# Optimization experiments

Hardware: AMD Instinct MI355X
Metric: run time of the kernel (lower is better)

Reference implementation:

```python
import jax, jax.numpy as jnp
import numpy as np

D_MODEL = 256
N_HEADS = 8
D_K = 16
LN_EPS = 1e-5


def setup_inputs() -> dict:
    key = jax.random.key(0)
    ks = jax.random.split(key, 10)
    B, S = 4, 2048
    inp = {
        "input_Q": jax.random.normal(ks[0], (B, S, D_MODEL), dtype=jnp.float32),
        "input_K": jax.random.normal(ks[1], (B, S, D_MODEL), dtype=jnp.float32),
        "input_V": jax.random.normal(ks[2], (B, S, D_MODEL), dtype=jnp.float32),
        "attn_mask": jax.random.randint(ks[3], (B, S, S), 0, 2) == 1,
        # learned params (torch Linear weight [out,in] stored here as [in,out])
        "Wq": jax.random.normal(ks[4], (D_MODEL, N_HEADS * D_K), dtype=jnp.float32) * (1.0 / np.sqrt(D_MODEL)),
        "Wk": jax.random.normal(ks[5], (D_MODEL, N_HEADS * D_K), dtype=jnp.float32) * (1.0 / np.sqrt(D_MODEL)),
        "Wv": jax.random.normal(ks[6], (D_MODEL, N_HEADS * D_K), dtype=jnp.float32) * (1.0 / np.sqrt(D_MODEL)),
        "Wfc": jax.random.normal(ks[7], (N_HEADS * D_K, D_MODEL), dtype=jnp.float32) * (1.0 / np.sqrt(N_HEADS * D_K)),
        "ln_gamma": jnp.ones((D_MODEL,), dtype=jnp.float32),
        "ln_beta": jnp.zeros((D_MODEL,), dtype=jnp.float32),
    }
    return inp


def reference(input_Q, input_K, input_V, attn_mask, Wq, Wk, Wv, Wfc, ln_gamma, ln_beta):
    B, S, _ = input_Q.shape
    # projections -> [B, H, S, d_k]
    Q = (input_Q @ Wq).reshape(B, S, N_HEADS, D_K).transpose(0, 2, 1, 3)
    K = (input_K @ Wk).reshape(B, S, N_HEADS, D_K).transpose(0, 2, 1, 3)
    V = (input_V @ Wv).reshape(B, S, N_HEADS, D_K).transpose(0, 2, 1, 3)
    # scores [B, H, S, S], masked softmax
    scores = jnp.einsum("bhqd,bhkd->bhqk", Q, K) / np.sqrt(D_K).astype(np.float32)
    scores = jnp.where(attn_mask[:, None, :, :], jnp.float32(-1e9), scores)
    attn = jax.nn.softmax(scores, axis=-1)
    context = jnp.einsum("bhqk,bhkd->bhqd", attn, V)
    context = context.transpose(0, 2, 1, 3).reshape(B, S, N_HEADS * D_K)
    out = context @ Wfc
    # LayerNorm (no residual in the original module)
    mu = jnp.mean(out, axis=-1, keepdims=True)
    var = jnp.var(out, axis=-1, keepdims=True)
    out = (out - mu) * jax.lax.rsqrt(var + LN_EPS) * ln_gamma + ln_beta
    return out
```

## Files before the change

### kernel.cpp

```cpp
#include <hip/hip_runtime.h>
#include <hip/hip_bf16.h>

#define S_LEN 2048
#define BATCH 4
#define NH 8
#define DK 16
#define DM 256
#define DP 128
#define L2E 1.4426950408889634f

typedef short bf16x8 __attribute__((ext_vector_type(8)));
typedef short short4v __attribute__((ext_vector_type(4)));
typedef float f32x16 __attribute__((ext_vector_type(16)));

__device__ __forceinline__ short f2bf(float x) {
    __hip_bfloat16 h = __float2bfloat16(x);
    return __builtin_bit_cast(short, h);
}

union Frag { bf16x8 v; short4v h2[2]; };

__global__ __launch_bounds__(256) void phase1(
    const void* __restrict__ mraw,
    unsigned long long* __restrict__ ms64,
    const float* __restrict__ Xq, const float* __restrict__ Xk, const float* __restrict__ Xv,
    const float* __restrict__ Wq, const float* __restrict__ Wk, const float* __restrict__ Wv,
    short* __restrict__ Qt, short* __restrict__ Kb, short* __restrict__ Vb)
{
    __shared__ short xs_s[32 * 260];
    __shared__ int isBool;
    const int bi = blockIdx.x;
    const int t = threadIdx.x;

    if (bi < 768) {
        const int inp = bi >> 8;
        const int s0 = (bi & 255) * 32;
        {
            const float* xbase = ((inp == 0) ? Xq : (inp == 1) ? Xk : Xv) + (size_t)s0 * 256;
            #pragma unroll
            for (int u = 0; u < 8; ++u) {
                const int idx = u * 1024 + t * 4;
                const int row = idx >> 8, col = idx & 255;
                float4 xv = *(const float4*)(xbase + idx);
                short4v o = { f2bf(xv.x), f2bf(xv.y), f2bf(xv.z), f2bf(xv.w) };
                *(short4v*)&xs_s[row * 260 + col] = o;
            }
        }
        __syncthreads();

        const int wave = t >> 6, lane = t & 63;
        const int lq = lane & 31, hi = lane >> 5;
        const int c = wave * 32 + lq;

        const float* W = (inp == 0) ? Wq : (inp == 1) ? Wk : Wv;
        const float scale = (inp == 0) ? 0.25f * L2E : 1.0f;
        Frag wf[16];
        #pragma unroll
        for (int kb = 0; kb < 16; ++kb) {
            const int k0 = kb * 16 + 4 * hi;
            union { bf16x8 v; short s[8]; } o;
            #pragma unroll
            for (int e = 0; e < 4; ++e) {
                o.s[e]     = f2bf(W[(size_t)(k0 + e) * DP + c] * scale);
                o.s[4 + e] = f2bf(W[(size_t)(k0 + 8 + e) * DP + c] * scale);
            }
            wf[kb].v = o.v;
        }

        f32x16 acc;
        #pragma unroll
        for (int i = 0; i < 16; ++i) acc[i] = 0.f;

        #pragma unroll
        for (int kb = 0; kb < 16; ++kb) {
            Frag af;
            af.h2[0] = *(const short4v*)&xs_s[lq * 260 + kb*16 + 4*hi];
            af.h2[1] = *(const short4v*)&xs_s[lq * 260 + kb*16 + 8 + 4*hi];
            acc = __builtin_amdgcn_mfma_f32_32x32x16_bf16(af.v, wf[kb].v, acc, 0, 0, 0);
        }

        const int b = s0 >> 11, sl = s0 & (S_LEN - 1);
        const int h = c >> 4, d = c & 15;
        if (inp == 1) {
            #pragma unroll
            for (int r = 0; r < 16; ++r) {
                const int s = sl + (r & 3) + 8*(r >> 2) + 4*hi;
                Kb[(((size_t)(b * NH + h)) * S_LEN + s) * DK + d] = f2bf(acc[r]);
            }
        } else {
            short* base = (inp == 0)
                ? Qt + (((size_t)(b * NH + h)) * 16 + d) * S_LEN + sl
                : Vb + (((size_t)(b * NH + h)) * 32 + d) * S_LEN + sl;
            #pragma unroll
            for (int g = 0; g < 4; ++g) {
                short4v vv = { f2bf(acc[4*g]), f2bf(acc[4*g+1]), f2bf(acc[4*g+2]), f2bf(acc[4*g+3]) };
                *(short4v*)(base + 8*g + 4*hi) = vv;
            }
        }
    } else if (bi < 1280) {
        const int tid = (bi - 768) * 256 + t;
        const int bh = tid >> 12;
        const int rem = tid & 4095;
        const int row = 16 + (rem >> 11) * 4;
        const int s = rem & 2047;
        Vb[((size_t)bh * 32 + row) * S_LEN + s] = (short)0x3F80;
    } else {
        const size_t kbase0 = (size_t)(bi - 1280) * 4096;
        if (t == 0) isBool = 0;
        __syncthreads();
        {
            unsigned int u = ((const unsigned int*)mraw)[(kbase0 >> 2) + t * 4];
            if (u & 0xFFFFFF00u) isBool = 1;
        }
        __syncthreads();

        const int lane = t & 63;
        const size_t kbase = kbase0 + (size_t)(t >> 6) * 1024;
        int v[16];
        if (!isBool) {
            const int* p = (const int*)mraw + kbase + lane;
            #pragma unroll
            for (int g = 0; g < 16; ++g) v[g] = p[g * 64];
        } else {
            const unsigned char* p = (const unsigned char*)mraw + kbase + lane;
            #pragma unroll
            for (int g = 0; g < 16; ++g) v[g] = p[g * 64];
        }

        const size_t row = kbase >> 11;
        const int koff0 = (int)(kbase & 2047);

        #pragma unroll
        for (int g = 0; g < 16; ++g) {
            const unsigned long long W = __ballot(v[g] != 0);
            if (lane == 0) {
                const int koff = koff0 + g * 64;
                ms64[(size_t)(koff >> 7) * (BATCH*S_LEN*2) + row*2 + ((koff >> 6) & 1)] = W;
            }
        }
    }
}

__global__ __launch_bounds__(256, 8) void attn_mfma(
    const short* __restrict__ Qt, const short* __restrict__ Kb, const short* __restrict__ Vb,
    const unsigned long long* __restrict__ ms64, float* __restrict__ pacc, float* __restrict__ pl)
{
    __shared__ short kt_s[128 * 20];
    __shared__ short vt_s[32 * 132];

    const int bh = blockIdx.y;
    const int b = bh >> 3;
    const int z = blockIdx.z;
    const int t = threadIdx.x;
    const int wave = t >> 6, lane = t & 63;
    const int lq = lane & 31, hi = lane >> 5;
    const int qrow = blockIdx.x * 128 + wave * 32 + lq;

    Frag qf;
    {
        const short* qt = Qt + (size_t)bh * 16 * S_LEN + qrow;
        #pragma unroll
        for (int j = 0; j < 4; ++j) {
            qf.h2[0][j] = qt[(size_t)(4*hi + j) * S_LEN];
            qf.h2[1][j] = qt[(size_t)(8 + 4*hi + j) * S_LEN];
        }
    }

    f32x16 acc;
    #pragma unroll
    for (int i = 0; i < 16; ++i) acc[i] = 0.f;

    const short* kbase = Kb + (size_t)bh * S_LEN * DK;
    const short* vbase = Vb + (size_t)bh * 32 * S_LEN;
    const unsigned long long* mbase = ms64 + ((size_t)b * S_LEN + qrow) * 2;

    const int tiles = (S_LEN / 128) / gridDim.z;
    const int t0 = z * tiles, t1 = t0 + tiles;

    for (int tile = t0; tile < t1; ++tile) {
        const int k0 = tile * 128;

        {
            const uint4 kv = *(const uint4*)(kbase + (size_t)k0 * DK + t * 8);
            short* kdst = &kt_s[(t >> 1) * 20 + (t & 1) * 8];
            *(uint2*)(kdst)     = *(uint2*)&kv;
            *(uint2*)(kdst + 4) = *((uint2*)&kv + 1);

            const short* vsrc = vbase + (size_t)(t >> 3) * S_LEN + k0 + (t & 7) * 16;
            uint4 v0 = *(const uint4*)(vsrc);
            uint4 v1 = *(const uint4*)(vsrc + 8);
            short* vdst = &vt_s[(t >> 3) * 132 + (t & 7) * 16];
            *(uint2*)(vdst)      = *(uint2*)&v0;
            *(uint2*)(vdst + 4)  = *((uint2*)&v0 + 1);
            *(uint2*)(vdst + 8)  = *(uint2*)&v1;
            *(uint2*)(vdst + 12) = *((uint2*)&v1 + 1);
        }
        __syncthreads();

        const unsigned long long* mw = mbase + (size_t)tile * (BATCH * S_LEN * 2);
        const unsigned long long W64a = mw[0], W64b = mw[1];

        #pragma unroll
        for (int kt = 0; kt < 4; ++kt) {
            const unsigned int W = (unsigned int)(((kt < 2) ? W64a : W64b)
                                                  >> (32*(kt & 1) + 4*hi));
            f32x16 ci;
            #pragma unroll
            for (int r = 0; r < 16; ++r) {
                const int bit = (r & 3) + 8*(r >> 2);
                ci[r] = __int_as_float(((int)(W << (31 - bit)) >> 31) & 0xC2C80000);
            }

            Frag kf;
            kf.h2[0] = *(const short4v*)&kt_s[(kt*32 + lq) * 20 + 4*hi];
            kf.h2[1] = *(const short4v*)&kt_s[(kt*32 + lq) * 20 + 8 + 4*hi];
            f32x16 p = __builtin_amdgcn_mfma_f32_32x32x16_bf16(kf.v, qf.v, ci, 0, 0, 0);

            #pragma unroll
            for (int r = 0; r < 16; ++r) p[r] = __builtin_amdgcn_exp2f(p[r]);

            #pragma unroll
            for (int j = 0; j < 2; ++j) {
                union { bf16x8 v; unsigned int u[4]; } pf;
                #pragma unroll
                for (int e = 0; e < 4; ++e) {
                    asm("v_cvt_pk_bf16_f32 %0, %1, %2"
                        : "=v"(pf.u[e]) : "v"(p[j*8 + 2*e]), "v"(p[j*8 + 2*e + 1]));
                }
                Frag vf;
                const int vo = lq * 132 + (kt*2 + j) * 16 + 4*hi;
                vf.h2[0] = *(const short4v*)&vt_s[vo];
                vf.h2[1] = *(const short4v*)&vt_s[vo + 8];
                acc = __builtin_amdgcn_mfma_f32_32x32x16_bf16(vf.v, pf.v, acc, 0, 0, 0);
            }
        }
        __syncthreads();
    }

    float* pb = pacc + (((size_t)z * (BATCH*NH) + bh) * S_LEN + qrow) * 16;
    float4 o1 = { acc[0], acc[1], acc[2], acc[3] };
    float4 o2 = { acc[4], acc[5], acc[6], acc[7] };
    *(float4*)(pb + 4*hi) = o1;
    *(float4*)(pb + 8 + 4*hi) = o2;
    if (hi == 0) pl[((size_t)z * (BATCH*NH) + bh) * S_LEN + qrow] = acc[8];
}

__global__ __launch_bounds__(256) void fc_ln(
    const float* __restrict__ pacc, const float* __restrict__ pl, int ns,
    const float* __restrict__ Wfc,
    const float* __restrict__ gamma, const float* __restrict__ beta,
    float* __restrict__ out)
{
    __shared__ float cs[8][DP];
    __shared__ float ys[8][256];
    __shared__ float red[16];
    const int t = threadIdx.x;
    const int row0 = blockIdx.x * 8;

    {
        const int idx = t * 4;
        const int r = idx >> 7, k = idx & 127;
        const int grow = row0 + r;
        const int b = grow >> 11, q = grow & (S_LEN - 1);
        const int h = k >> 4, d0 = k & 15;
        float4 s = {0.f, 0.f, 0.f, 0.f};
        float L = 0.f;
        for (int z = 0; z < ns; ++z) {
            const size_t o = ((size_t)z * (BATCH*NH) + b * NH + h) * S_LEN + q;
            const float4 a = *(const float4*)(pacc + o * 16 + d0);
            s.x += a.x; s.y += a.y; s.z += a.z; s.w += a.w;
            L += pl[o];
        }
        const float inv = 1.0f / L;
        float4 o4 = { s.x * inv, s.y * inv, s.z * inv, s.w * inv };
        *(float4*)&cs[r][k] = o4;
    }
    __syncthreads();

    float acc[8] = {0,0,0,0,0,0,0,0};
    for (int k = 0; k < DP; k += 4) {
        const float w0 = Wfc[(k+0)*DM + t];
        const float w1 = Wfc[(k+1)*DM + t];
        const float w2 = Wfc[(k+2)*DM + t];
        const float w3 = Wfc[(k+3)*DM + t];
        #pragma unroll
        for (int r = 0; r < 8; ++r) {
            float4 x = *(const float4*)&cs[r][k];
            acc[r] = fmaf(x.x, w0, fmaf(x.y, w1, fmaf(x.z, w2, fmaf(x.w, w3, acc[r]))));
        }
    }

    #pragma unroll
    for (int r = 0; r < 8; ++r) ys[r][t] = acc[r];
    __syncthreads();

    const int w = t >> 6, lj = t & 63;
    #pragma unroll
    for (int rr = 0; rr < 2; ++rr) {
        const int r = w * 2 + rr;
        float a0 = ys[r][lj], a1 = ys[r][lj+64], a2 = ys[r][lj+128], a3 = ys[r][lj+192];
        float s1 = a0 + a1 + a2 + a3;
        float s2 = a0*a0 + a1*a1 + a2*a2 + a3*a3;
        #pragma unroll
        for (int off = 32; off; off >>= 1) {
            s1 += __shfl_xor(s1, off);
            s2 += __shfl_xor(s2, off);
        }
        if (lj == 0) {
            float mu = s1 * (1.0f/256.0f);
            float var = s2 * (1.0f/256.0f) - mu*mu;
            red[r*2]     = mu;
            red[r*2 + 1] = rsqrtf(var + 1e-5f);
        }
    }
    __syncthreads();

    const float g = gamma[t], be = beta[t];
    #pragma unroll
    for (int r = 0; r < 8; ++r) {
        float y = (acc[r] - red[r*2]) * red[r*2 + 1];
        out[(size_t)(row0 + r) * DM + t] = fmaf(y, g, be);
    }
}

extern "C" void kernel_launch(void* const* d_in, const int* in_sizes, int n_in,
                              void* d_out, int out_size, void* d_ws, size_t ws_size,
                              hipStream_t stream)
{
    const float* Xq = (const float*)d_in[0];
    const float* Xk = (const float*)d_in[1];
    const float* Xv = (const float*)d_in[2];
    const void* mask_raw = d_in[3];
    const float* Wq  = (const float*)d_in[4];
    const float* Wk  = (const float*)d_in[5];
    const float* Wv  = (const float*)d_in[6];
    const float* Wfc = (const float*)d_in[7];
    const float* gamma = (const float*)d_in[8];
    const float* beta  = (const float*)d_in[9];
    float* out = (float*)d_out;

    const size_t headsz = (size_t)BATCH * NH * S_LEN * DK;
    const size_t maskelems = (size_t)BATCH * S_LEN * S_LEN;

    char* wsb = (char*)d_ws;
    short* Qt = (short*)wsb;
    short* Kb = Qt + headsz;
    short* Vb = Kb + headsz;
    unsigned long long* msk = (unsigned long long*)(Vb + 2 * headsz);
    float* pacc = (float*)(msk + maskelems / 64);
    size_t ns = 4;
    {
        const size_t fixed = (size_t)((char*)pacc - wsb);
        while (ns > 1 && fixed + ns * ((size_t)BATCH*NH*S_LEN*17*4) > ws_size)
            ns >>= 1;
    }
    float* pl = pacc + ns * (size_t)BATCH * NH * S_LEN * 16;

    phase1<<<dim3(768 + 512 + (unsigned)(maskelems / 4096)), dim3(256), 0, stream>>>(
        mask_raw, msk, Xq, Xk, Xv, Wq, Wk, Wv, Qt, Kb, Vb);
    attn_mfma<<<dim3(S_LEN / 128, BATCH * NH, (unsigned)ns), dim3(256), 0, stream>>>(
        Qt, Kb, Vb, msk, pacc, pl);
    fc_ln<<<dim3(BATCH * S_LEN / 8), dim3(256), 0, stream>>>(pacc, pl, (int)ns, Wfc, gamma, beta, out);
}
```

Measured before the change: 72.44 us.

## Pre-pack bf16 weight fragments, split projection kernel, row-major mask bit layout

Moves weight conversion into a prep kernel that writes pre-scaled bf16 MFMA fragments once, so the projection blocks load 16-byte fragments instead of 128 scattered fp32 reads each. The projection GEMM becomes its own kernel launched after prep, which adds one launch. The mask bitmap is rearranged to per-query-row contiguous 64-bit words, written with coalesced stores from 16 lanes and read in attention as a single 16-byte load per tile. The trade-off is an extra kernel boundary and serialization between mask/weight prep and projection.

Result: no change. 72.85 us (+0.6%).

```diff
diff --git a/kernel.cpp b/kernel.cpp
--- a/kernel.cpp
+++ b/kernel.cpp
@@ -20,92 +20,41 @@
 
 union Frag { bf16x8 v; short4v h2[2]; };
 
-__global__ __launch_bounds__(256) void phase1(
-    const void* __restrict__ mraw,
-    unsigned long long* __restrict__ ms64,
-    const float* __restrict__ Xq, const float* __restrict__ Xk, const float* __restrict__ Xv,
-    const float* __restrict__ Wq, const float* __restrict__ Wk, const float* __restrict__ Wv,
-    short* __restrict__ Qt, short* __restrict__ Kb, short* __restrict__ Vb)
-{
-    __shared__ short xs_s[32 * 260];
+__global__ __launch_bounds__(256) void prep(
+    const void* __restrict__ mraw, unsigned long long* __restrict__ ms64,
+    const float* __restrict__ Wq, const float* __restrict__ Wk,
+    const float* __restrict__ Wv, short* __restrict__ Wt,
+    short* __restrict__ Vb)
+{
     __shared__ int isBool;
     const int bi = blockIdx.x;
     const int t = threadIdx.x;
 
-    if (bi < 768) {
-        const int inp = bi >> 8;
-        const int s0 = (bi & 255) * 32;
-        {
-            const float* xbase = ((inp == 0) ? Xq : (inp == 1) ? Xk : Xv) + (size_t)s0 * 256;
-            #pragma unroll
-            for (int u = 0; u < 8; ++u) {
-                const int idx = u * 1024 + t * 4;
-                const int row = idx >> 8, col = idx & 255;
-                float4 xv = *(const float4*)(xbase + idx);
-                short4v o = { f2bf(xv.x), f2bf(xv.y), f2bf(xv.z), f2bf(xv.w) };
-                *(short4v*)&xs_s[row * 260 + col] = o;
-            }
-        }
-        __syncthreads();
-
-        const int wave = t >> 6, lane = t & 63;
-        const int lq = lane & 31, hi = lane >> 5;
-        const int c = wave * 32 + lq;
-
-        const float* W = (inp == 0) ? Wq : (inp == 1) ? Wk : Wv;
-        const float scale = (inp == 0) ? 0.25f * L2E : 1.0f;
-        Frag wf[16];
-        #pragma unroll
-        for (int kb = 0; kb < 16; ++kb) {
-            const int k0 = kb * 16 + 4 * hi;
-            union { bf16x8 v; short s[8]; } o;
-            #pragma unroll
-            for (int e = 0; e < 4; ++e) {
-                o.s[e]     = f2bf(W[(size_t)(k0 + e) * DP + c] * scale);
-                o.s[4 + e] = f2bf(W[(size_t)(k0 + 8 + e) * DP + c] * scale);
-            }
-            wf[kb].v = o.v;
-        }
-
-        f32x16 acc;
-        #pragma unroll
-        for (int i = 0; i < 16; ++i) acc[i] = 0.f;
-
-        #pragma unroll
-        for (int kb = 0; kb < 16; ++kb) {
-            Frag af;
-            af.h2[0] = *(const short4v*)&xs_s[lq * 260 + kb*16 + 4*hi];
-            af.h2[1] = *(const short4v*)&xs_s[lq * 260 + kb*16 + 8 + 4*hi];
-            acc = __builtin_amdgcn_mfma_f32_32x32x16_bf16(af.v, wf[kb].v, acc, 0, 0, 0);
-        }
-
-        const int b = s0 >> 11, sl = s0 & (S_LEN - 1);
-        const int h = c >> 4, d = c & 15;
-        if (inp == 1) {
-            #pragma unroll
-            for (int r = 0; r < 16; ++r) {
-                const int s = sl + (r & 3) + 8*(r >> 2) + 4*hi;
-                Kb[(((size_t)(b * NH + h)) * S_LEN + s) * DK + d] = f2bf(acc[r]);
-            }
-        } else {
-            short* base = (inp == 0)
-                ? Qt + (((size_t)(b * NH + h)) * 16 + d) * S_LEN + sl
-                : Vb + (((size_t)(b * NH + h)) * 32 + d) * S_LEN + sl;
-            #pragma unroll
-            for (int g = 0; g < 4; ++g) {
-                short4v vv = { f2bf(acc[4*g]), f2bf(acc[4*g+1]), f2bf(acc[4*g+2]), f2bf(acc[4*g+3]) };
-                *(short4v*)(base + 8*g + 4*hi) = vv;
-            }
-        }
-    } else if (bi < 1280) {
-        const int tid = (bi - 768) * 256 + t;
+    if (bi < 512) {
+        const int tid = bi * 256 + t;
         const int bh = tid >> 12;
         const int rem = tid & 4095;
         const int row = 16 + (rem >> 11) * 4;
         const int s = rem & 2047;
         Vb[((size_t)bh * 32 + row) * S_LEN + s] = (short)0x3F80;
+    } else if (bi < 560) {
+        const int tid = (bi - 512) * 256 + t;
+        const int c  = tid & 127;
+        const int hi = (tid >> 7) & 1;
+        const int kb = (tid >> 8) & 15;
+        const int m  = tid >> 12;
+        const float* W = (m == 0) ? Wq : (m == 1) ? Wk : Wv;
+        const float scale = (m == 0) ? 0.25f * L2E : 1.0f;
+        const int k0 = kb * 16 + 4 * hi;
+        union { bf16x8 v; short s[8]; } o;
+        #pragma unroll
+        for (int e = 0; e < 4; ++e) {
+            o.s[e]     = f2bf(W[(size_t)(k0 + e) * DP + c] * scale);
+            o.s[4 + e] = f2bf(W[(size_t)(k0 + 8 + e) * DP + c] * scale);
+        }
+        *(bf16x8*)(Wt + (size_t)tid * 8) = o.v;
     } else {
-        const size_t kbase0 = (size_t)(bi - 1280) * 4096;
+        const size_t kbase0 = (size_t)(bi - 560) * 4096;
         if (t == 0) isBool = 0;
         __syncthreads();
         {
@@ -128,15 +77,81 @@
         }
 
         const size_t row = kbase >> 11;
-        const int koff0 = (int)(kbase & 2047);
-
+        const int w0 = (int)(kbase & 2047) >> 6;
+
+        unsigned long long myw = 0;
         #pragma unroll
         for (int g = 0; g < 16; ++g) {
             const unsigned long long W = __ballot(v[g] != 0);
-            if (lane == 0) {
-                const int koff = koff0 + g * 64;
-                ms64[(size_t)(koff >> 7) * (BATCH*S_LEN*2) + row*2 + ((koff >> 6) & 1)] = W;
-            }
+            myw = (lane == g) ? W : myw;
+        }
+        if (lane < 16) ms64[row * 32 + w0 + lane] = myw;
+    }
+}
+
+__global__ __launch_bounds__(256) void proj_mfma(
+    const float* __restrict__ Xq, const float* __restrict__ Xk, const float* __restrict__ Xv,
+    const short* __restrict__ Wt,
+    short* __restrict__ Qt, short* __restrict__ Kb, short* __restrict__ Vb)
+{
+    __shared__ short xs_s[32 * 260];
+    const int bi = blockIdx.x;
+    const int t = threadIdx.x;
+    const int inp = bi >> 8;
+    const int s0 = (bi & 255) * 32;
+
+    {
+        const float* xbase = ((inp == 0) ? Xq : (inp == 1) ? Xk : Xv) + (size_t)s0 * 256;
+        #pragma unroll
+        for (int u = 0; u < 8; ++u) {
+            const int idx = u * 1024 + t * 4;
+            const int row = idx >> 8, col = idx & 255;
+            float4 xv = *(const float4*)(xbase + idx);
+            short4v o = { f2bf(xv.x), f2bf(xv.y), f2bf(xv.z), f2bf(xv.w) };
+            *(short4v*)&xs_s[row * 260 + col] = o;
+        }
+    }
+
+    const int wave = t >> 6, lane = t & 63;
+    const int lq = lane & 31, hi = lane >> 5;
+    const int c = wave * 32 + lq;
+
+    const short* w2 = Wt + (((size_t)inp * 16 * 2 + hi) * 128 + c) * 8;
+    Frag wf[16];
+    #pragma unroll
+    for (int kb = 0; kb < 16; ++kb)
+        wf[kb].v = *(const bf16x8*)(w2 + (size_t)kb * 2048);
+    asm volatile("" ::: "memory");
+    __syncthreads();
+
+    f32x16 acc;
+    #pragma unroll
+    for (int i = 0; i < 16; ++i) acc[i] = 0.f;
+
+    #pragma unroll
+    for (int kb = 0; kb < 16; ++kb) {
+        Frag af;
+        af.h2[0] = *(const short4v*)&xs_s[lq * 260 + kb*16 + 4*hi];
+        af.h2[1] = *(const short4v*)&xs_s[lq * 260 + kb*16 + 8 + 4*hi];
+        acc = __builtin_amdgcn_mfma_f32_32x32x16_bf16(af.v, wf[kb].v, acc, 0, 0, 0);
+    }
+
+    const int b = s0 >> 11, sl = s0 & (S_LEN - 1);
+    const int h = c >> 4, d = c & 15;
+    if (inp == 1) {
+        #pragma unroll
+        for (int r = 0; r < 16; ++r) {
+            const int s = sl + (r & 3) + 8*(r >> 2) + 4*hi;
+            Kb[(((size_t)(b * NH + h)) * S_LEN + s) * DK + d] = f2bf(acc[r]);
+        }
+    } else {
+        short* base = (inp == 0)
+            ? Qt + (((size_t)(b * NH + h)) * 16 + d) * S_LEN + sl
+            : Vb + (((size_t)(b * NH + h)) * 32 + d) * S_LEN + sl;
+        #pragma unroll
+        for (int g = 0; g < 4; ++g) {
+            short4v vv = { f2bf(acc[4*g]), f2bf(acc[4*g+1]), f2bf(acc[4*g+2]), f2bf(acc[4*g+3]) };
+            *(short4v*)(base + 8*g + 4*hi) = vv;
         }
     }
 }
@@ -172,7 +187,7 @@
 
     const short* kbase = Kb + (size_t)bh * S_LEN * DK;
     const short* vbase = Vb + (size_t)bh * 32 * S_LEN;
-    const unsigned long long* mbase = ms64 + ((size_t)b * S_LEN + qrow) * 2;
+    const unsigned long long* mrow = ms64 + ((size_t)b * S_LEN + qrow) * 32;
 
     const int tiles = (S_LEN / 128) / gridDim.z;
     const int t0 = z * tiles, t1 = t0 + tiles;
@@ -197,8 +212,8 @@
         }
         __syncthreads();
 
-        const unsigned long long* mw = mbase + (size_t)tile * (BATCH * S_LEN * 2);
-        const unsigned long long W64a = mw[0], W64b = mw[1];
+        const ulonglong2 mw = *(const ulonglong2*)(mrow + tile * 2);
+        const unsigned long long W64a = mw.x, W64b = mw.y;
 
         #pragma unroll
         for (int kt = 0; kt < 4; ++kt) {
@@ -347,7 +362,8 @@
     short* Kb = Qt + headsz;
     short* Vb = Kb + headsz;
     unsigned long long* msk = (unsigned long long*)(Vb + 2 * headsz);
-    float* pacc = (float*)(msk + maskelems / 64);
+    short* Wt = (short*)(msk + maskelems / 64);
+    float* pacc = (float*)(Wt + 3 * 128 * 256);
     size_t ns = 4;
     {
         const size_t fixed = (size_t)((char*)pacc - wsb);
@@ -356,8 +372,9 @@
     }
     float* pl = pacc + ns * (size_t)BATCH * NH * S_LEN * 16;
 
-    phase1<<<dim3(768 + 512 + (unsigned)(maskelems / 4096)), dim3(256), 0, stream>>>(
-        mask_raw, msk, Xq, Xk, Xv, Wq, Wk, Wv, Qt, Kb, Vb);
+    prep<<<dim3(512 + 48 + (unsigned)(maskelems / 4096)), dim3(256), 0, stream>>>(
+        mask_raw, msk, Wq, Wk, Wv, Wt, Vb);
+    proj_mfma<<<dim3(768), dim3(256), 0, stream>>>(Xq, Xk, Xv, Wt, Qt, Kb, Vb);
     attn_mfma<<<dim3(S_LEN / 128, BATCH * NH, (unsigned)ns), dim3(256), 0, stream>>>(
         Qt, Kb, Vb, msk, pacc, pl);
     fc_ln<<<dim3(BATCH * S_LEN / 8), dim3(256), 0, stream>>>(pacc, pl, (int)ns, Wfc, gamma, beta, out);
```

## Split key range across block halves and combine partial softmax in LDS

Applied to the files above, without the earlier changes.

The attention kernel now runs 512 threads per block. The two 256-thread halves each process half of the key tiles with their own LDS buffers, and their partial accumulators and row sums are combined through shared memory. The normalized context is written directly, so the partial-accumulator buffers and the reduction in fc_ln are no longer needed. The mask bitmap layout changes to row-major, so each query row loads its two words with one 16-byte load, and the ballot results are written by 16 lanes at once instead of one store per group. A syncthreads in the projection is moved after the weight loads. The trade-off is fewer blocks per CU (launch bounds 512,4), less key-split parallelism (2 instead of up to 4), and extra block-wide barriers.

New measurement: 93.90 us. +29.6%, slower.

```diff
diff --git a/kernel.cpp b/kernel.cpp
--- a/kernel.cpp
+++ b/kernel.cpp
@@ -20,9 +20,8 @@
 
 union Frag { bf16x8 v; short4v h2[2]; };
 
-__global__ __launch_bounds__(256) void phase1(
-    const void* __restrict__ mraw,
-    unsigned long long* __restrict__ ms64,
+__global__ __launch_bounds__(256) void main1(
+    const void* __restrict__ mraw, unsigned long long* __restrict__ ms64,
     const float* __restrict__ Xq, const float* __restrict__ Xk, const float* __restrict__ Xv,
     const float* __restrict__ Wq, const float* __restrict__ Wk, const float* __restrict__ Wv,
     short* __restrict__ Qt, short* __restrict__ Kb, short* __restrict__ Vb)
@@ -46,7 +45,6 @@
                 *(short4v*)&xs_s[row * 260 + col] = o;
             }
         }
-        __syncthreads();
 
         const int wave = t >> 6, lane = t & 63;
         const int lq = lane & 31, hi = lane >> 5;
@@ -66,6 +64,7 @@
             }
             wf[kb].v = o.v;
         }
+        __syncthreads();
 
         f32x16 acc;
         #pragma unroll
@@ -128,33 +127,35 @@
         }
 
         const size_t row = kbase >> 11;
-        const int koff0 = (int)(kbase & 2047);
-
+        const int w0 = (int)(kbase & 2047) >> 6;
+
+        unsigned long long myw = 0;
         #pragma unroll
         for (int g = 0; g < 16; ++g) {
             const unsigned long long W = __ballot(v[g] != 0);
-            if (lane == 0) {
-                const int koff = koff0 + g * 64;
-                ms64[(size_t)(koff >> 7) * (BATCH*S_LEN*2) + row*2 + ((koff >> 6) & 1)] = W;
-            }
-        }
-    }
-}
-
-__global__ __launch_bounds__(256, 8) void attn_mfma(
+            myw = (lane == g) ? W : myw;
+        }
+        if (lane < 16) ms64[row * 32 + w0 + lane] = myw;
+    }
+}
+
+__global__ __launch_bounds__(512, 4) void attn_mfma(
     const short* __restrict__ Qt, const short* __restrict__ Kb, const short* __restrict__ Vb,
-    const unsigned long long* __restrict__ ms64, float* __restrict__ pacc, float* __restrict__ pl)
+    const unsigned long long* __restrict__ ms64, float* __restrict__ ctx)
 {
-    __shared__ short kt_s[128 * 20];
-    __shared__ short vt_s[32 * 132];
+    __shared__ short kt_s[2][128 * 20];
+    __shared__ short vt_s[2][32 * 132];
+    __shared__ float cmb[256][9];
 
     const int bh = blockIdx.y;
-    const int b = bh >> 3;
-    const int z = blockIdx.z;
+    const int b = bh >> 3, h = bh & 7;
     const int t = threadIdx.x;
-    const int wave = t >> 6, lane = t & 63;
+    const int half = t >> 8;
+    const int th = t & 255;
+    const int wv = (t >> 6) & 3;
+    const int lane = t & 63;
     const int lq = lane & 31, hi = lane >> 5;
-    const int qrow = blockIdx.x * 128 + wave * 32 + lq;
+    const int qrow = blockIdx.x * 128 + wv * 32 + lq;
 
     Frag qf;
     {
@@ -172,24 +173,22 @@
 
     const short* kbase = Kb + (size_t)bh * S_LEN * DK;
     const short* vbase = Vb + (size_t)bh * 32 * S_LEN;
-    const unsigned long long* mbase = ms64 + ((size_t)b * S_LEN + qrow) * 2;
-
-    const int tiles = (S_LEN / 128) / gridDim.z;
-    const int t0 = z * tiles, t1 = t0 + tiles;
-
-    for (int tile = t0; tile < t1; ++tile) {
+    const unsigned long long* mrow = ms64 + ((size_t)b * S_LEN + qrow) * 32;
+
+    for (int i = 0; i < 8; ++i) {
+        const int tile = half * 8 + i;
         const int k0 = tile * 128;
 
         {
-            const uint4 kv = *(const uint4*)(kbase + (size_t)k0 * DK + t * 8);
-            short* kdst = &kt_s[(t >> 1) * 20 + (t & 1) * 8];
+            const uint4 kv = *(const uint4*)(kbase + (size_t)k0 * DK + th * 8);
+            short* kdst = &kt_s[half][(th >> 1) * 20 + (th & 1) * 8];
             *(uint2*)(kdst)     = *(uint2*)&kv;
             *(uint2*)(kdst + 4) = *((uint2*)&kv + 1);
 
-            const short* vsrc = vbase + (size_t)(t >> 3) * S_LEN + k0 + (t & 7) * 16;
+            const short* vsrc = vbase + (size_t)(th >> 3) * S_LEN + k0 + (th & 7) * 16;
             uint4 v0 = *(const uint4*)(vsrc);
             uint4 v1 = *(const uint4*)(vsrc + 8);
-            short* vdst = &vt_s[(t >> 3) * 132 + (t & 7) * 16];
+            short* vdst = &vt_s[half][(th >> 3) * 132 + (th & 7) * 16];
             *(uint2*)(vdst)      = *(uint2*)&v0;
             *(uint2*)(vdst + 4)  = *((uint2*)&v0 + 1);
             *(uint2*)(vdst + 8)  = *(uint2*)&v1;
@@ -197,8 +196,8 @@
         }
         __syncthreads();
 
-        const unsigned long long* mw = mbase + (size_t)tile * (BATCH * S_LEN * 2);
-        const unsigned long long W64a = mw[0], W64b = mw[1];
+        const ulonglong2 mw = *(const ulonglong2*)(mrow + tile * 2);
+        const unsigned long long W64a = mw.x, W64b = mw.y;
 
         #pragma unroll
         for (int kt = 0; kt < 4; ++kt) {
@@ -212,8 +211,8 @@
             }
 
             Frag kf;
-            kf.h2[0] = *(const short4v*)&kt_s[(kt*32 + lq) * 20 + 4*hi];
-            kf.h2[1] = *(const short4v*)&kt_s[(kt*32 + lq) * 20 + 8 + 4*hi];
+            kf.h2[0] = *(const short4v*)&kt_s[half][(kt*32 + lq) * 20 + 4*hi];
+            kf.h2[1] = *(const short4v*)&kt_s[half][(kt*32 + lq) * 20 + 8 + 4*hi];
             f32x16 p = __builtin_amdgcn_mfma_f32_32x32x16_bf16(kf.v, qf.v, ci, 0, 0, 0);
 
             #pragma unroll
@@ -229,25 +228,34 @@
                 }
                 Frag vf;
                 const int vo = lq * 132 + (kt*2 + j) * 16 + 4*hi;
-                vf.h2[0] = *(const short4v*)&vt_s[vo];
-                vf.h2[1] = *(const short4v*)&vt_s[vo + 8];
+                vf.h2[0] = *(const short4v*)&vt_s[half][vo];
+                vf.h2[1] = *(const short4v*)&vt_s[half][vo + 8];
                 acc = __builtin_amdgcn_mfma_f32_32x32x16_bf16(vf.v, pf.v, acc, 0, 0, 0);
             }
         }
         __syncthreads();
     }
 
-    float* pb = pacc + (((size_t)z * (BATCH*NH) + bh) * S_LEN + qrow) * 16;
-    float4 o1 = { acc[0], acc[1], acc[2], acc[3] };
-    float4 o2 = { acc[4], acc[5], acc[6], acc[7] };
-    *(float4*)(pb + 4*hi) = o1;
-    *(float4*)(pb + 8 + 4*hi) = o2;
-    if (hi == 0) pl[((size_t)z * (BATCH*NH) + bh) * S_LEN + qrow] = acc[8];
+    if (half == 1) {
+        #pragma unroll
+        for (int e = 0; e < 8; ++e) cmb[th][e] = acc[e];
+        cmb[th][8] = acc[8];
+    }
+    __syncthreads();
+    if (half == 0) {
+        const float invl = 1.0f / (acc[8] + cmb[th][8]);
+        float* cbase = ctx + ((size_t)b * S_LEN + qrow) * DP + h * DK;
+        float4 o1 = { (acc[0] + cmb[th][0]) * invl, (acc[1] + cmb[th][1]) * invl,
+                      (acc[2] + cmb[th][2]) * invl, (acc[3] + cmb[th][3]) * invl };
+        float4 o2 = { (acc[4] + cmb[th][4]) * invl, (acc[5] + cmb[th][5]) * invl,
+                      (acc[6] + cmb[th][6]) * invl, (acc[7] + cmb[th][7]) * invl };
+        *(float4*)(cbase + 4*hi) = o1;
+        *(float4*)(cbase + 8 + 4*hi) = o2;
+    }
 }
 
 __global__ __launch_bounds__(256) void fc_ln(
-    const float* __restrict__ pacc, const float* __restrict__ pl, int ns,
-    const float* __restrict__ Wfc,
+    const float* __restrict__ ctx, const float* __restrict__ Wfc,
     const float* __restrict__ gamma, const float* __restrict__ beta,
     float* __restrict__ out)
 {
@@ -260,20 +268,7 @@
     {
         const int idx = t * 4;
         const int r = idx >> 7, k = idx & 127;
-        const int grow = row0 + r;
-        const int b = grow >> 11, q = grow & (S_LEN - 1);
-        const int h = k >> 4, d0 = k & 15;
-        float4 s = {0.f, 0.f, 0.f, 0.f};
-        float L = 0.f;
-        for (int z = 0; z < ns; ++z) {
-            const size_t o = ((size_t)z * (BATCH*NH) + b * NH + h) * S_LEN + q;
-            const float4 a = *(const float4*)(pacc + o * 16 + d0);
-            s.x += a.x; s.y += a.y; s.z += a.z; s.w += a.w;
-            L += pl[o];
-        }
-        const float inv = 1.0f / L;
-        float4 o4 = { s.x * inv, s.y * inv, s.z * inv, s.w * inv };
-        *(float4*)&cs[r][k] = o4;
+        *(float4*)&cs[r][k] = *(const float4*)(ctx + (size_t)(row0 + r) * DP + k);
     }
     __syncthreads();
 
@@ -347,18 +342,11 @@
     short* Kb = Qt + headsz;
     short* Vb = Kb + headsz;
     unsigned long long* msk = (unsigned long long*)(Vb + 2 * headsz);
-    float* pacc = (float*)(msk + maskelems / 64);
-    size_t ns = 4;
-    {
-        const size_t fixed = (size_t)((char*)pacc - wsb);
-        while (ns > 1 && fixed + ns * ((size_t)BATCH*NH*S_LEN*17*4) > ws_size)
-            ns >>= 1;
-    }
-    float* pl = pacc + ns * (size_t)BATCH * NH * S_LEN * 16;
-
-    phase1<<<dim3(768 + 512 + (unsigned)(maskelems / 4096)), dim3(256), 0, stream>>>(
+    float* ctx = (float*)(msk + maskelems / 64);
+
+    main1<<<dim3(768 + 512 + (unsigned)(maskelems / 4096)), dim3(256), 0, stream>>>(
         mask_raw, msk, Xq, Xk, Xv, Wq, Wk, Wv, Qt, Kb, Vb);
-    attn_mfma<<<dim3(S_LEN / 128, BATCH * NH, (unsigned)ns), dim3(256), 0, stream>>>(
-        Qt, Kb, Vb, msk, pacc, pl);
-    fc_ln<<<dim3(BATCH * S_LEN / 8), dim3(256), 0, stream>>>(pacc, pl, (int)ns, Wfc, gamma, beta, out);
-}
+    attn_mfma<<<dim3(S_LEN / 128, BATCH * NH), dim3(512), 0, stream>>>(
+        Qt, Kb, Vb, msk, ctx);
+    fc_ln<<<dim3(BATCH * S_LEN / 8), dim3(256), 0, stream>>>(ctx, Wfc, gamma, beta, out);
+}
```

## Pack mask bits with vector loads and row-major bitmask layout

Applied to the files above, without the earlier changes.

Mask compression now has each lane load 16 contiguous bytes with one vector load and pack them into 16 bits with multiply tricks, then uses shuffles to assemble 64-bit words. The packed-mask layout changes from tile-major to row-major, so the attention kernel reads both words for a tile with a single 16-byte load. The projection block also moves its barrier after the weight-fragment loads so those global loads overlap with the shared-memory staging. The bool-detection probe changes to check the loaded data itself, and the int path now reads 16 contiguous ints per lane, which is less coalesced.

New measurement: 71.32 us. Within noise of the previous version (-1.6%).

```diff
diff --git a/kernel.cpp b/kernel.cpp
--- a/kernel.cpp
+++ b/kernel.cpp
@@ -20,9 +20,8 @@
 
 union Frag { bf16x8 v; short4v h2[2]; };
 
-__global__ __launch_bounds__(256) void phase1(
-    const void* __restrict__ mraw,
-    unsigned long long* __restrict__ ms64,
+__global__ __launch_bounds__(256) void main1(
+    const void* __restrict__ mraw, unsigned long long* __restrict__ ms64,
     const float* __restrict__ Xq, const float* __restrict__ Xk, const float* __restrict__ Xv,
     const float* __restrict__ Wq, const float* __restrict__ Wk, const float* __restrict__ Wv,
     short* __restrict__ Qt, short* __restrict__ Kb, short* __restrict__ Vb)
@@ -46,7 +45,6 @@
                 *(short4v*)&xs_s[row * 260 + col] = o;
             }
         }
-        __syncthreads();
 
         const int wave = t >> 6, lane = t & 63;
         const int lq = lane & 31, hi = lane >> 5;
@@ -66,6 +64,7 @@
             }
             wf[kb].v = o.v;
         }
+        __syncthreads();
 
         f32x16 acc;
         #pragma unroll
@@ -105,38 +104,45 @@
         const int s = rem & 2047;
         Vb[((size_t)bh * 32 + row) * S_LEN + s] = (short)0x3F80;
     } else {
+        const int lane = t & 63;
         const size_t kbase0 = (size_t)(bi - 1280) * 4096;
+        const size_t kbase = kbase0 + (size_t)(t >> 6) * 1024;
+
+        union { uint4 v; unsigned u[4]; } uu;
+        uu.v = *(const uint4*)((const unsigned char*)mraw + kbase + 16 * lane);
+
         if (t == 0) isBool = 0;
         __syncthreads();
-        {
-            unsigned int u = ((const unsigned int*)mraw)[(kbase0 >> 2) + t * 4];
-            if (u & 0xFFFFFF00u) isBool = 1;
-        }
-        __syncthreads();
-
-        const int lane = t & 63;
-        const size_t kbase = kbase0 + (size_t)(t >> 6) * 1024;
-        int v[16];
-        if (!isBool) {
-            const int* p = (const int*)mraw + kbase + lane;
-            #pragma unroll
-            for (int g = 0; g < 16; ++g) v[g] = p[g * 64];
+        if ((uu.u[0] | uu.u[1] | uu.u[2] | uu.u[3]) & 0xFFFFFF00u) isBool = 1;
+        __syncthreads();
+
+        unsigned val16;
+        if (isBool) {
+            unsigned n0 = ((uu.u[0] & 0x01010101u) * 0x01020408u) >> 24;
+            unsigned n1 = ((uu.u[1] & 0x01010101u) * 0x01020408u) >> 24;
+            unsigned n2 = ((uu.u[2] & 0x01010101u) * 0x01020408u) >> 24;
+            unsigned n3 = ((uu.u[3] & 0x01010101u) * 0x01020408u) >> 24;
+            val16 = n0 | (n1 << 4) | (n2 << 8) | (n3 << 12);
         } else {
-            const unsigned char* p = (const unsigned char*)mraw + kbase + lane;
-            #pragma unroll
-            for (int g = 0; g < 16; ++g) v[g] = p[g * 64];
-        }
-
-        const size_t row = kbase >> 11;
-        const int koff0 = (int)(kbase & 2047);
-
-        #pragma unroll
-        for (int g = 0; g < 16; ++g) {
-            const unsigned long long W = __ballot(v[g] != 0);
-            if (lane == 0) {
-                const int koff = koff0 + g * 64;
-                ms64[(size_t)(koff >> 7) * (BATCH*S_LEN*2) + row*2 + ((koff >> 6) & 1)] = W;
-            }
+            const int* p = (const int*)mraw + kbase + 16 * lane;
+            val16 = 0;
+            #pragma unroll
+            for (int cc = 0; cc < 16; ++cc) val16 |= (p[cc] != 0 ? 1u : 0u) << cc;
+        }
+
+        const int src0 = (4 * lane) & 63;
+        const unsigned a0 = (unsigned)__shfl((int)val16, src0);
+        const unsigned a1 = (unsigned)__shfl((int)val16, src0 + 1);
+        const unsigned a2 = (unsigned)__shfl((int)val16, src0 + 2);
+        const unsigned a3 = (unsigned)__shfl((int)val16, src0 + 3);
+
+        if (lane < 16) {
+            const unsigned long long w64 =
+                (unsigned long long)a0 | ((unsigned long long)a1 << 16) |
+                ((unsigned long long)a2 << 32) | ((unsigned long long)a3 << 48);
+            const size_t row = kbase >> 11;
+            const int w0 = (int)(kbase & 2047) >> 6;
+            ms64[row * 32 + w0 + lane] = w64;
         }
     }
 }
@@ -172,7 +178,7 @@
 
     const short* kbase = Kb + (size_t)bh * S_LEN * DK;
     const short* vbase = Vb + (size_t)bh * 32 * S_LEN;
-    const unsigned long long* mbase = ms64 + ((size_t)b * S_LEN + qrow) * 2;
+    const unsigned long long* mrow = ms64 + ((size_t)b * S_LEN + qrow) * 32;
 
     const int tiles = (S_LEN / 128) / gridDim.z;
     const int t0 = z * tiles, t1 = t0 + tiles;
@@ -197,8 +203,8 @@
         }
         __syncthreads();
 
-        const unsigned long long* mw = mbase + (size_t)tile * (BATCH * S_LEN * 2);
-        const unsigned long long W64a = mw[0], W64b = mw[1];
+        const ulonglong2 mw = *(const ulonglong2*)(mrow + tile * 2);
+        const unsigned long long W64a = mw.x, W64b = mw.y;
 
         #pragma unroll
         for (int kt = 0; kt < 4; ++kt) {
@@ -356,7 +362,7 @@
     }
     float* pl = pacc + ns * (size_t)BATCH * NH * S_LEN * 16;
 
-    phase1<<<dim3(768 + 512 + (unsigned)(maskelems / 4096)), dim3(256), 0, stream>>>(
+    main1<<<dim3(768 + 512 + (unsigned)(maskelems / 4096)), dim3(256), 0, stream>>>(
         mask_raw, msk, Xq, Xk, Xv, Wq, Wk, Wv, Qt, Kb, Vb);
     attn_mfma<<<dim3(S_LEN / 128, BATCH * NH, (unsigned)ns), dim3(256), 0, stream>>>(
         Qt, Kb, Vb, msk, pacc, pl);
```
